# Kernel optimization log

Hardware: AMD Instinct MI355X
Metric: run time of the kernel (lower is better)

Reference implementation:

```python
import jax, jax.numpy as jnp
import numpy as np

B, S = 4, 1024
D = 256          # token_dim = channel_dim = expert_dim
D_LF = 768       # longformer hidden size
ADAPT = 128
NEXP = 4
HID = 64
DSUM = 3 * D + D_LF  # combiner concat width = 1536


def _gelu(v):
    return jax.nn.gelu(v, approximate=False)  # torch nn.GELU default = exact


def setup_inputs() -> dict:
    key = jax.random.key(0)
    ks = iter(jax.random.split(key, 40))
    def w(shape, scale=1.0):
        return jax.random.normal(next(ks), shape, jnp.float32) * scale
    z = lambda *shape: jnp.zeros(shape, jnp.float32)
    return dict(
        x=w((B, S, D)),
        lf_out=w((B, S, D_LF)),
        W_feat=w((D, ADAPT), D ** -0.5), b_feat=z(ADAPT),
        Wt=w((D, D), D ** -0.5), bt=z(D),
        Wt_a=w((ADAPT, D * D), 0.01 * ADAPT ** -0.5), bt_a=z(D * D),
        Wc=w((D, D), D ** -0.5), bc=z(D),
        Wc_a=w((ADAPT, D * D), 0.01 * ADAPT ** -0.5), bc_a=z(D * D),
        We=w((NEXP, D, D), D ** -0.5), be=z(NEXP, D),
        We_a=w((NEXP, ADAPT, D * D), 0.01 * ADAPT ** -0.5), be_a=z(NEXP, D * D),
        Wg=w((ADAPT, NEXP + 1), ADAPT ** -0.5), bg=z(NEXP + 1),
        Wphi=w((D, HID)), bphi=z(D, HID),
        Wpsi1=w((D * HID, HID), (D * HID) ** -0.5), bpsi1=z(HID),
        Wpsi2=w((HID, D), HID ** -0.5), bpsi2=z(D),
        Wres=w((DSUM, DSUM), DSUM ** -0.5), bres=z(DSUM),
        W1=w((DSUM, HID), DSUM ** -0.5), b1=z(HID),
        W2=w((HID, 4), HID ** -0.5), b2=z(4),
        Wo=w((DSUM, D), DSUM ** -0.5), bo=z(D),
    )


def reference(x, lf_out, W_feat, b_feat, Wt, bt, Wt_a, bt_a, Wc, bc, Wc_a, bc_a,
              We, be, We_a, be_a, Wg, bg, Wphi, bphi, Wpsi1, bpsi1, Wpsi2, bpsi2,
              Wres, bres, W1, b1, W2, b2, Wo, bo):
    Bx, Sx, d = x.shape
    N = Bx * Sx
    xf = x.reshape(N, d)
    lff = lf_out.reshape(N, -1)
    # featurizer -> per-token adapt features; global mean drives adaptive weights
    adapt = xf @ W_feat + b_feat            # [N, ADAPT]
    am = adapt.mean(axis=0)                 # [ADAPT] single adapt vector (LiquidLinear view constraint)

    def liquid(inp, Wb, bb, Wa, ba):
        Wdyn = Wb + (am @ Wa + ba).reshape(Wb.shape)
        return inp @ Wdyn + bb

    tok = liquid(xf, Wt, bt, Wt_a, bt_a)    # [N, D] token mixer
    chan = liquid(xf, Wc, bc, Wc_a, bc_a)   # [N, D] channel mixer

    # MixtureOfExperts: softmax gate over NEXP liquid experts + 1 KA expert
    gate = jax.nn.softmax(adapt @ Wg + bg, axis=-1)              # [N, NEXP+1]
    dW = (jnp.einsum('a,eaf->ef', am, We_a) + be_a).reshape(We.shape)
    eo = jnp.einsum('nd,edo->neo', xf, We + dW) + be[None]       # [N, E, D]
    # Kolmogorov-Arnold expert: per-feature phi (Linear(1,HID)+gelu), then psi MLP
    phi = _gelu(xf[:, :, None] * Wphi[None] + bphi[None])        # [N, D, HID]
    ka = _gelu(phi.reshape(N, -1) @ Wpsi1 + bpsi1) @ Wpsi2 + bpsi2
    moe = jnp.einsum('ne,ned->nd', gate[:, :-1], eo) + gate[:, -1:] * ka

    # ComponentCombination: learned softmax component weights + residual path
    concat = jnp.concatenate([tok, chan, moe, lff], axis=-1)     # [N, DSUM]
    residual = concat @ Wres + bres
    h = _gelu(concat @ W1 + b1)
    cw = jax.nn.softmax(h @ W2 + b2, axis=-1)                    # [N, 4]
    combined = jnp.concatenate(
        [cw[:, 0:1] * tok, cw[:, 1:2] * chan, cw[:, 2:3] * moe, cw[:, 3:4] * lff],
        axis=-1) + residual                                      # [N, DSUM]
    return (combined @ Wo + bo).reshape(Bx, Sx, d)
```

## Files before the change

### kernel.cpp

```cpp
#include <hip/hip_runtime.h>
#include <hip/hip_bf16.h>


__device__ __forceinline__ float gelu_f(float v){ return 0.5f*v*(1.0f + erff(v*0.70710678118654752f)); }

__device__ __forceinline__ float u16tof(unsigned short u){
  union { unsigned int i; float f; } v; v.i = ((unsigned int)u) << 16; return v.f;
}
__device__ __forceinline__ unsigned short f2b(float f){
  union { float f; unsigned int u; } v; v.f = f;
  unsigned int r = v.u + 0x7fffu + ((v.u >> 16) & 1u);
  return (unsigned short)(r >> 16);
}

using short8  = __attribute__((ext_vector_type(8))) short;
using float4v = __attribute__((ext_vector_type(4))) float;

template<int MODE>
__global__ __launch_bounds__(256) void mgemm_k(
    const unsigned short* __restrict__ A, const unsigned short* __restrict__ Bt,
    const float* __restrict__ bias, float* __restrict__ C,
    int M, int N, int K, long sB, long sBias, long sC)
{
  if constexpr (MODE==1){
    Bt   += sB   * blockIdx.z;
    bias += sBias* blockIdx.z;
    C    += sC   * blockIdx.z;
  }
  __shared__ __align__(16) unsigned short As[128][40];
  __shared__ __align__(16) unsigned short Bs[128][40];
  const int tid  = threadIdx.x;
  const int m0   = blockIdx.y*128, n0 = blockIdx.x*128;
  const int wave = tid>>6, lane = tid&63;
  const int wm   = (wave&1)*64, wn = (wave>>1)*64;
  const int q    = lane>>4, r = lane&15;
  const int sm   = tid>>2, sq = (tid&3)*8;

  float4v acc[4][4];
  #pragma unroll
  for (int i=0;i<4;i++)
    #pragma unroll
    for (int j=0;j<4;j++) acc[i][j] = (float4v){0.f,0.f,0.f,0.f};

  const unsigned short* Ap = A + (long)(m0+sm)*K + sq;
  const unsigned short* Bp = Bt + (long)(n0+sm)*K + sq;
  const long rstep = (long)64*K;

  for (int k0 = 0; k0 < K; k0 += 32){
    uint4 a0 = *(const uint4*)(Ap + k0);
    uint4 a1 = *(const uint4*)(Ap + k0 + rstep);
    uint4 b0 = *(const uint4*)(Bp + k0);
    uint4 b1 = *(const uint4*)(Bp + k0 + rstep);
    __syncthreads();
    *(uint4*)&As[sm   ][sq] = a0;
    *(uint4*)&As[sm+64][sq] = a1;
    *(uint4*)&Bs[sm   ][sq] = b0;
    *(uint4*)&Bs[sm+64][sq] = b1;
    __syncthreads();
    short8 af[4], bf[4];
    #pragma unroll
    for (int mt=0;mt<4;mt++) af[mt] = *(const short8*)&As[wm + mt*16 + r][q*8];
    #pragma unroll
    for (int nt=0;nt<4;nt++) bf[nt] = *(const short8*)&Bs[wn + nt*16 + r][q*8];
    #pragma unroll
    for (int mt=0;mt<4;mt++)
      #pragma unroll
      for (int nt=0;nt<4;nt++)
        acc[mt][nt] = __builtin_amdgcn_mfma_f32_16x16x32_bf16(af[mt], bf[nt], acc[mt][nt], 0, 0, 0);
  }

  #pragma unroll
  for (int nt=0;nt<4;nt++){
    int col = n0 + wn + nt*16 + r;
    float bb = bias[col];
    #pragma unroll
    for (int mt=0;mt<4;mt++){
      #pragma unroll
      for (int i=0;i<4;i++){
        int row = m0 + wm + mt*16 + q*4 + i;
        C[(long)row*N + col] = acc[mt][nt][i] + bb;
      }
    }
  }
}

__global__ __launch_bounds__(256) void cvtb_k(const float* __restrict__ in, unsigned short* __restrict__ out){
  int i = (blockIdx.x*256 + threadIdx.x)*4;
  float4 v = *(const float4*)(in + i);
  ushort4 o; o.x = f2b(v.x); o.y = f2b(v.y); o.z = f2b(v.z); o.w = f2b(v.w);
  *(ushort4*)(out + i) = o;
}

__global__ __launch_bounds__(256) void tconv_k(const float* __restrict__ in, unsigned short* __restrict__ out, int R, int C){
  __shared__ float t[64][65];
  const int tid = threadIdx.x;
  const int c0 = blockIdx.x*64, r0 = blockIdx.y*64;
  const int lr = tid>>2, lc0 = (tid&3)*16;
  #pragma unroll
  for (int i=0;i<4;i++){
    float4 v = *(const float4*)&in[(long)(r0+lr)*C + c0 + lc0 + i*4];
    t[lr][lc0+i*4+0]=v.x; t[lr][lc0+i*4+1]=v.y; t[lr][lc0+i*4+2]=v.z; t[lr][lc0+i*4+3]=v.w;
  }
  __syncthreads();
  const int oc = tid>>2, os = (tid&3)*16;
  #pragma unroll
  for (int i=0;i<16;i++)
    out[(long)(c0+oc)*R + r0 + os + i] = f2b(t[os+i][oc]);
}

__device__ __forceinline__ float4 ld4(const float* p){ return *(const float4*)p; }
__device__ __forceinline__ float4 ld4(const unsigned short* p){
  ushort4 u = *(const ushort4*)p;
  return make_float4(u16tof(u.x), u16tof(u.y), u16tof(u.z), u16tof(u.w));
}
template<typename AT, int MODE>
__global__ __launch_bounds__(256) void gemm_k(
    const AT* __restrict__ A, const float* __restrict__ B, const float* __restrict__ bias,
    float* __restrict__ C, int M, int N, int K, int Kc)
{
  int klo = 0, khi = K;
  if constexpr (MODE==2){ klo = blockIdx.z*Kc; khi = klo + Kc; }
  __shared__ __align__(16) float As[16][68];
  __shared__ __align__(16) float Bs[16][68];
  const int tid = threadIdx.x;
  const int m0 = blockIdx.y*64, n0 = blockIdx.x*64;
  const int ty = tid>>4, tx = tid&15;
  const int ar = tid>>2, ac = (tid&3)*4;
  const int kr = tid>>4, nc = (tid&15)*4;
  float acc[4][4] = {};
  const AT* Ap = A + (long)(m0+ar)*K;

  for (int k0 = klo; k0 < khi; k0 += 16){
    float4 av = ld4(Ap + k0 + ac);
    float4 bv = *(const float4*)(B + (long)(k0+kr)*N + (n0+nc));
    __syncthreads();
    As[ac+0][ar] = av.x; As[ac+1][ar] = av.y; As[ac+2][ar] = av.z; As[ac+3][ar] = av.w;
    *(float4*)&Bs[kr][nc] = bv;
    __syncthreads();
    #pragma unroll
    for (int k = 0; k < 16; k++){
      float4 a4 = *(const float4*)&As[k][ty*4];
      float4 b4 = *(const float4*)&Bs[k][tx*4];
      float a[4] = {a4.x,a4.y,a4.z,a4.w};
      float b[4] = {b4.x,b4.y,b4.z,b4.w};
      #pragma unroll
      for (int i = 0; i < 4; i++)
        #pragma unroll
        for (int j = 0; j < 4; j++)
          acc[i][j] = fmaf(a[i], b[j], acc[i][j]);
    }
  }
  float bv4[4];
  #pragma unroll
  for (int j = 0; j < 4; j++) bv4[j] = bias[n0 + tx*4 + j];
  #pragma unroll
  for (int i = 0; i < 4; i++){
    long row = m0 + ty*4 + i;
    #pragma unroll
    for (int j = 0; j < 4; j++){
      float v = acc[i][j];
      if constexpr (MODE==2){
        if (blockIdx.z == 0) v += bv4[j];
        atomicAdd(&C[row*(long)N + n0 + tx*4 + j], v);
      } else {
        C[row*(long)N + n0 + tx*4 + j] = v + bv4[j];
      }
    }
  }
}

__global__ __launch_bounds__(256) void colmean_k(const float* __restrict__ adapt, float* __restrict__ am){
  __shared__ float red[256];
  int a = blockIdx.x, tid = threadIdx.x;
  float s = 0.f;
  for (int n = tid; n < 4096; n += 256) s += adapt[n*128 + a];
  red[tid] = s; __syncthreads();
  for (int w = 128; w > 0; w >>= 1){ if (tid < w) red[tid] += red[tid+w]; __syncthreads(); }
  if (tid == 0) am[a] = red[0] * (1.0f/4096.0f);
}

__global__ __launch_bounds__(256) void gate_k(const float* __restrict__ adapt,
    const float* __restrict__ Wg, const float* __restrict__ bg, float* __restrict__ gate){
  __shared__ float wg[640]; __shared__ float bgs[5];
  int tid = threadIdx.x;
  for (int i = tid; i < 640; i += 256) wg[i] = Wg[i];
  if (tid < 5) bgs[tid] = bg[tid];
  __syncthreads();
  int n = blockIdx.x*256 + tid;
  float l[5] = {bgs[0],bgs[1],bgs[2],bgs[3],bgs[4]};
  const float* ar = adapt + (long)n*128;
  for (int a = 0; a < 128; a++){
    float av = ar[a];
    #pragma unroll
    for (int e = 0; e < 5; e++) l[e] = fmaf(av, wg[a*5+e], l[e]);
  }
  float mx = l[0];
  #pragma unroll
  for (int e = 1; e < 5; e++) mx = fmaxf(mx, l[e]);
  float sum = 0.f;
  #pragma unroll
  for (int e = 0; e < 5; e++){ l[e] = expf(l[e]-mx); sum += l[e]; }
  float inv = 1.0f/sum;
  #pragma unroll
  for (int e = 0; e < 5; e++) gate[(long)n*5+e] = l[e]*inv;
}

__global__ __launch_bounds__(256) void dynw_k(const float* __restrict__ am,
    const float* Wt, const float* Wt_a, const float* bt_a,
    const float* Wc, const float* Wc_a, const float* bc_a,
    const float* We, const float* We_a, const float* be_a,
    unsigned short* __restrict__ Wdyn_t)
{
  __shared__ float ams[128];
  int tid = threadIdx.x;
  if (tid < 128) ams[tid] = am[tid];
  __syncthreads();
  long gid = (long)blockIdx.x*256 + tid;
  int seg = (int)(gid >> 16); int m = (int)(gid & 65535);
  const float *W, *Wa, *ba;
  if (seg == 0){ W = Wt; Wa = Wt_a; ba = bt_a; }
  else if (seg == 1){ W = Wc; Wa = Wc_a; ba = bc_a; }
  else { int e = seg-2; W = We + (long)e*65536; Wa = We_a + (long)e*65536*128; ba = be_a + (long)e*65536; }
  float s = W[m] + ba[m];
  for (int a = 0; a < 128; a++) s = fmaf(ams[a], Wa[(long)a*65536 + m], s);
  int row = m >> 8, col = m & 255;
  Wdyn_t[(long)seg*65536 + (long)col*256 + row] = f2b(s);
}

__global__ void bias6_k(const float* bt, const float* bc, const float* be, float* bias6){
  int z = blockIdx.x, t = threadIdx.x;
  const float* s = (z==0) ? bt : (z==1) ? bc : be + (long)(z-2)*256;
  bias6[z*256 + t] = s[t];
}

__global__ __launch_bounds__(256) void psi1_k(const float* __restrict__ xf,
    const float* __restrict__ Wphi, const float* __restrict__ bphi,
    const float* __restrict__ Wpsi1, float* __restrict__ h1)
{
  __shared__ __align__(16) float xs[64][33];
  __shared__ __align__(16) float As[64][68];
  __shared__ __align__(16) float Bs[64][68];
  const int tid = threadIdx.x;
  const int m0 = blockIdx.x*64;
  const int d_lo = blockIdx.y*32;
  {
    int t = tid>>2, dq = (tid&3)*8;
    const float* src = xf + (long)(m0+t)*256 + d_lo + dq;
    #pragma unroll
    for (int i = 0; i < 8; i++) xs[t][dq+i] = src[i];
  }
  const int ty = tid>>4, tx = tid&15;
  const int k_a = tid>>2, t0_a = (tid&3)*16;
  float acc[4][4] = {};
  __syncthreads();
  for (int dd = 0; dd < 32; dd++){
    int d = d_lo + dd;
    const float* wp = Wpsi1 + (long)d*4096;
    float w  = Wphi[d*64 + k_a];
    float bb = bphi[d*64 + k_a];
    __syncthreads();
    #pragma unroll
    for (int i = 0; i < 16; i++){
      int idx = tid + 256*i;
      Bs[idx>>6][idx&63] = wp[idx];
    }
    #pragma unroll
    for (int i = 0; i < 16; i++){
      float xv = xs[t0_a+i][dd];
      As[k_a][t0_a+i] = gelu_f(fmaf(xv, w, bb));
    }
    __syncthreads();
    #pragma unroll
    for (int kk = 0; kk < 64; kk++){
      float4 a4 = *(const float4*)&As[kk][ty*4];
      float4 b4 = *(const float4*)&Bs[kk][tx*4];
      float a[4] = {a4.x,a4.y,a4.z,a4.w};
      float b[4] = {b4.x,b4.y,b4.z,b4.w};
      #pragma unroll
      for (int i = 0; i < 4; i++)
        #pragma unroll
        for (int j = 0; j < 4; j++)
          acc[i][j] = fmaf(a[i], b[j], acc[i][j]);
    }
  }
  #pragma unroll
  for (int i = 0; i < 4; i++)
    #pragma unroll
    for (int j = 0; j < 4; j++)
      atomicAdd(&h1[(long)(m0 + ty*4 + i)*64 + tx*4 + j], acc[i][j]);
}

__global__ __launch_bounds__(256) void h1g_k(const float* __restrict__ h1,
    const float* __restrict__ bpsi1, float* __restrict__ h1g){
  int i = blockIdx.x*256 + threadIdx.x;
  h1g[i] = gelu_f(h1[i] + bpsi1[i & 63]);
}

__global__ __launch_bounds__(256) void concat_k(const float* __restrict__ tok,
    const float* __restrict__ chan, const float* __restrict__ eo,
    const float* __restrict__ gate, const float* __restrict__ ka,
    const float* __restrict__ lf, unsigned short* __restrict__ concat)
{
  int n = blockIdx.x, tid = threadIdx.x;
  const float* g = gate + (long)n*5;
  float g0=g[0], g1=g[1], g2=g[2], g3=g[3], g4=g[4];
  long nb = (long)n*1536;
  int d = tid;
  concat[nb + d]        = f2b(tok[(long)n*256 + d]);
  concat[nb + 256 + d]  = f2b(chan[(long)n*256 + d]);
  float m = g0*eo[(long)n*256 + d]
          + g1*eo[1048576 + (long)n*256 + d]
          + g2*eo[2097152 + (long)n*256 + d]
          + g3*eo[3145728 + (long)n*256 + d]
          + g4*ka[(long)n*256 + d];
  concat[nb + 512 + d] = f2b(m);
  for (int j = tid; j < 768; j += 256) concat[nb + 768 + j] = f2b(lf[(long)n*768 + j]);
}

__global__ __launch_bounds__(256) void cw_k(const float* __restrict__ hpre,
    const float* __restrict__ W2, const float* __restrict__ b2, float* __restrict__ cw){
  __shared__ float w2s[256]; __shared__ float b2s[4];
  int tid = threadIdx.x;
  w2s[tid] = W2[tid];
  if (tid < 4) b2s[tid] = b2[tid];
  __syncthreads();
  int n = blockIdx.x*256 + tid;
  float l[4] = {b2s[0],b2s[1],b2s[2],b2s[3]};
  const float* hp = hpre + (long)n*64;
  for (int j = 0; j < 64; j++){
    float hj = gelu_f(hp[j]);
    #pragma unroll
    for (int c = 0; c < 4; c++) l[c] = fmaf(hj, w2s[j*4+c], l[c]);
  }
  float mx = fmaxf(fmaxf(l[0],l[1]), fmaxf(l[2],l[3]));
  float sum = 0.f;
  #pragma unroll
  for (int c = 0; c < 4; c++){ l[c] = expf(l[c]-mx); sum += l[c]; }
  float inv = 1.0f/sum;
  #pragma unroll
  for (int c = 0; c < 4; c++) cw[(long)n*4+c] = l[c]*inv;
}

__global__ __launch_bounds__(256) void combine_k(unsigned short* __restrict__ concat,
    const float* __restrict__ residual, const float* __restrict__ cw){
  int n = blockIdx.x;
  int j = blockIdx.y*256 + threadIdx.x;
  int seg = (j < 768) ? (j >> 8) : 3;
  long idx = (long)n*1536 + j;
  float v = fmaf(cw[(long)n*4 + seg], u16tof(concat[idx]), residual[idx]);
  concat[idx] = f2b(v);
}

extern "C" void kernel_launch(void* const* d_in, const int* in_sizes, int n_in,
                              void* d_out, int out_size, void* d_ws, size_t ws_size,
                              hipStream_t stream)
{
  const float* x      = (const float*)d_in[0];
  const float* lf     = (const float*)d_in[1];
  const float* W_feat = (const float*)d_in[2];
  const float* b_feat = (const float*)d_in[3];
  const float* Wt     = (const float*)d_in[4];
  const float* bt     = (const float*)d_in[5];
  const float* Wt_a   = (const float*)d_in[6];
  const float* bt_a   = (const float*)d_in[7];
  const float* Wc     = (const float*)d_in[8];
  const float* bc     = (const float*)d_in[9];
  const float* Wc_a   = (const float*)d_in[10];
  const float* bc_a   = (const float*)d_in[11];
  const float* We     = (const float*)d_in[12];
  const float* be     = (const float*)d_in[13];
  const float* We_a   = (const float*)d_in[14];
  const float* be_a   = (const float*)d_in[15];
  const float* Wg     = (const float*)d_in[16];
  const float* bg     = (const float*)d_in[17];
  const float* Wphi   = (const float*)d_in[18];
  const float* bphi   = (const float*)d_in[19];
  const float* Wpsi1  = (const float*)d_in[20];
  const float* bpsi1  = (const float*)d_in[21];
  const float* Wpsi2  = (const float*)d_in[22];
  const float* bpsi2  = (const float*)d_in[23];
  const float* Wres   = (const float*)d_in[24];
  const float* bres   = (const float*)d_in[25];
  const float* W1     = (const float*)d_in[26];
  const float* b1     = (const float*)d_in[27];
  const float* W2     = (const float*)d_in[28];
  const float* b2     = (const float*)d_in[29];
  const float* Wo     = (const float*)d_in[30];
  const float* bo     = (const float*)d_in[31];

  float* ws = (float*)d_ws;
  float* T      = ws;
  float* tok    = T;
  float* chan   = T + 1048576;
  float* eo     = T + 2*1048576;
  float* adapt  = T + 6*1048576;
  float* am     = adapt + 524288;
  float* gate   = am + 128;
  float* bias6  = gate + 20480;
  float* h1     = bias6 + 1536;
  float* h1g    = h1 + 262144;
  float* ka     = h1g + 262144;
  unsigned short* xb     = (unsigned short*)(ka + 1048576);
  unsigned short* Wdyn_t = xb + 1048576;
  unsigned short* Wres_t = Wdyn_t + 393216;
  unsigned short* Wo_t   = Wres_t + 2359296;
  unsigned short* concat = Wo_t + 393216;
  float* residual = T;
  float* hpre   = adapt;
  float* cw     = adapt + 262144;

  dim3 b256(256);

  cvtb_k<<<dim3(1024), b256, 0, stream>>>(x, xb);
  tconv_k<<<dim3(24,24), b256, 0, stream>>>(Wres, Wres_t, 1536, 1536);
  tconv_k<<<dim3(4,24),  b256, 0, stream>>>(Wo,   Wo_t,   1536, 256);

  gemm_k<float,0><<<dim3(2,64,1), b256, 0, stream>>>(x, W_feat, b_feat, adapt, 4096,128,256, 0);

  colmean_k<<<dim3(128), b256, 0, stream>>>(adapt, am);
  gate_k<<<dim3(16), b256, 0, stream>>>(adapt, Wg, bg, gate);

  dynw_k<<<dim3(1536), b256, 0, stream>>>(am, Wt,Wt_a,bt_a, Wc,Wc_a,bc_a, We,We_a,be_a, Wdyn_t);
  bias6_k<<<dim3(6), b256, 0, stream>>>(bt, bc, be, bias6);

  mgemm_k<1><<<dim3(2,32,6), b256, 0, stream>>>(xb, Wdyn_t, bias6, T, 4096,256,256, 65536,256,1048576);

  hipMemsetAsync(h1, 0, 262144*sizeof(float), stream);
  psi1_k<<<dim3(64,8), b256, 0, stream>>>(x, Wphi, bphi, Wpsi1, h1);
  h1g_k<<<dim3(1024), b256, 0, stream>>>(h1, bpsi1, h1g);
  gemm_k<float,0><<<dim3(4,64,1), b256, 0, stream>>>(h1g, Wpsi2, bpsi2, ka, 4096,256,64, 0);

  concat_k<<<dim3(4096), b256, 0, stream>>>(tok, chan, eo, gate, ka, lf, concat);

  mgemm_k<0><<<dim3(12,32,1), b256, 0, stream>>>(concat, Wres_t, bres, residual, 4096,1536,1536, 0,0,0);

  hipMemsetAsync(hpre, 0, 262144*sizeof(float), stream);
  gemm_k<unsigned short,2><<<dim3(1,64,8), b256, 0, stream>>>(concat, W1, b1, hpre, 4096,64,1536, 192);
  cw_k<<<dim3(16), b256, 0, stream>>>(hpre, W2, b2, cw);

  combine_k<<<dim3(4096,6), b256, 0, stream>>>(concat, residual, cw);

  mgemm_k<0><<<dim3(2,32,1), b256, 0, stream>>>(concat, Wo_t, bo, (float*)d_out, 4096,256,1536, 0,0,0);
}
```

Baseline: 744.0 us.

## Move KA psi1 GEMM to bf16 MFMA with transposed bf16 weight

Replaces the fp32 FMA-based fused phi+psi1 kernel with one that runs the inner products on bf16 MFMA 16x16x32 instructions. The Wpsi1 weight is transposed and converted to bf16 in an extra tconv launch, and Wphi/bphi are packed as bf16 pairs in shared memory. Each thread computes its GELU phi values before the barrier, overlapping them with the global weight loads. This is meant to cut the ALU cost of the largest fp32 GEMM (K=16384). In exchange it adds a conversion pass over Wpsi1 and bf16 rounding of the activations, weights and phi parameters.

```diff
diff --git a/kernel.cpp b/kernel.cpp
--- a/kernel.cpp
+++ b/kernel.cpp
@@ -81,6 +81,105 @@
         C[(long)row*N + col] = acc[mt][nt][i] + bb;
       }
     }
+  }
+}
+
+__global__ __launch_bounds__(256) void psi1m_k(const float* __restrict__ x,
+    const float* __restrict__ Wphi, const float* __restrict__ bphi,
+    const unsigned short* __restrict__ Wpsi1_t, float* __restrict__ h1)
+{
+  __shared__ float xs[64][33];
+  __shared__ __align__(16) unsigned int wbls[32][64];
+  __shared__ __align__(16) unsigned short As[64][72];
+  __shared__ __align__(16) unsigned short Bs[64][72];
+  const int tid = threadIdx.x;
+  const int m0 = blockIdx.x*64, d_lo = blockIdx.y*32;
+
+  {
+    int m = tid>>2, off = (tid&3)*8;
+    const float* src = x + (long)(m0+m)*256 + d_lo + off;
+    #pragma unroll
+    for (int i=0;i<8;i++) xs[m][off+i] = src[i];
+  }
+  {
+    #pragma unroll
+    for (int i=0;i<2;i++){
+      int idx4 = tid + 256*i;
+      int rr = idx4>>4, cc = (idx4&15)*4;
+      float4 w4 = *(const float4*)&Wphi[(long)(d_lo+rr)*64 + cc];
+      float4 b4 = *(const float4*)&bphi[(long)(d_lo+rr)*64 + cc];
+      uint4 p;
+      p.x = (unsigned int)f2b(w4.x) | ((unsigned int)f2b(b4.x)<<16);
+      p.y = (unsigned int)f2b(w4.y) | ((unsigned int)f2b(b4.y)<<16);
+      p.z = (unsigned int)f2b(w4.z) | ((unsigned int)f2b(b4.z)<<16);
+      p.w = (unsigned int)f2b(w4.w) | ((unsigned int)f2b(b4.w)<<16);
+      *(uint4*)&wbls[rr][cc] = p;
+    }
+  }
+  const int wave = tid>>6, lane = tid&63;
+  const int wm = (wave&1)*32, wn = (wave>>1)*32;
+  const int q = lane>>4, r = lane&15;
+  const int pm = tid>>2, pk = (tid&3)*16;
+  const int bn = tid>>2, bk = (tid&3)*16;
+
+  float4v acc[2][2];
+  #pragma unroll
+  for (int i=0;i<2;i++)
+    #pragma unroll
+    for (int j=0;j<2;j++) acc[i][j] = (float4v){0.f,0.f,0.f,0.f};
+
+  __syncthreads();
+
+  for (int dd=0; dd<32; dd++){
+    int dglob = d_lo + dd;
+    const unsigned short* wp = Wpsi1_t + (long)bn*16384 + (long)dglob*64 + bk;
+    uint4 b0 = *(const uint4*)wp;
+    uint4 b1 = *(const uint4*)(wp + 8);
+    float xv = xs[pm][dd];
+    ushort4 ph[4];
+    #pragma unroll
+    for (int kk=0; kk<4; kk++){
+      uint4 wb = *(const uint4*)&wbls[dd][pk + kk*4];
+      unsigned int u[4] = {wb.x, wb.y, wb.z, wb.w};
+      unsigned short o[4];
+      #pragma unroll
+      for (int e=0;e<4;e++){
+        float w = u16tof((unsigned short)(u[e] & 0xffffu));
+        float b = u16tof((unsigned short)(u[e] >> 16));
+        o[e] = f2b(gelu_f(fmaf(xv, w, b)));
+      }
+      ph[kk].x=o[0]; ph[kk].y=o[1]; ph[kk].z=o[2]; ph[kk].w=o[3];
+    }
+    __syncthreads();
+    *(uint4*)&Bs[bn][bk]   = b0;
+    *(uint4*)&Bs[bn][bk+8] = b1;
+    #pragma unroll
+    for (int kk=0;kk<4;kk++) *(ushort4*)&As[pm][pk+kk*4] = ph[kk];
+    __syncthreads();
+    #pragma unroll
+    for (int kb=0; kb<2; kb++){
+      short8 af[2], bfr[2];
+      #pragma unroll
+      for (int mt=0;mt<2;mt++) af[mt]  = *(const short8*)&As[wm+mt*16+r][kb*32 + q*8];
+      #pragma unroll
+      for (int nt=0;nt<2;nt++) bfr[nt] = *(const short8*)&Bs[wn+nt*16+r][kb*32 + q*8];
+      #pragma unroll
+      for (int mt=0;mt<2;mt++)
+        #pragma unroll
+        for (int nt=0;nt<2;nt++)
+          acc[mt][nt] = __builtin_amdgcn_mfma_f32_16x16x32_bf16(af[mt], bfr[nt], acc[mt][nt], 0, 0, 0);
+    }
+  }
+  #pragma unroll
+  for (int nt=0;nt<2;nt++){
+    int col = wn + nt*16 + r;
+    #pragma unroll
+    for (int mt=0;mt<2;mt++)
+      #pragma unroll
+      for (int i=0;i<4;i++){
+        int row = m0 + wm + mt*16 + q*4 + i;
+        atomicAdd(&h1[(long)row*64 + col], acc[mt][nt][i]);
+      }
   }
 }
 
@@ -231,63 +330,6 @@
   int z = blockIdx.x, t = threadIdx.x;
   const float* s = (z==0) ? bt : (z==1) ? bc : be + (long)(z-2)*256;
   bias6[z*256 + t] = s[t];
-}
-
-__global__ __launch_bounds__(256) void psi1_k(const float* __restrict__ xf,
-    const float* __restrict__ Wphi, const float* __restrict__ bphi,
-    const float* __restrict__ Wpsi1, float* __restrict__ h1)
-{
-  __shared__ __align__(16) float xs[64][33];
-  __shared__ __align__(16) float As[64][68];
-  __shared__ __align__(16) float Bs[64][68];
-  const int tid = threadIdx.x;
-  const int m0 = blockIdx.x*64;
-  const int d_lo = blockIdx.y*32;
-  {
-    int t = tid>>2, dq = (tid&3)*8;
-    const float* src = xf + (long)(m0+t)*256 + d_lo + dq;
-    #pragma unroll
-    for (int i = 0; i < 8; i++) xs[t][dq+i] = src[i];
-  }
-  const int ty = tid>>4, tx = tid&15;
-  const int k_a = tid>>2, t0_a = (tid&3)*16;
-  float acc[4][4] = {};
-  __syncthreads();
-  for (int dd = 0; dd < 32; dd++){
-    int d = d_lo + dd;
-    const float* wp = Wpsi1 + (long)d*4096;
-    float w  = Wphi[d*64 + k_a];
-    float bb = bphi[d*64 + k_a];
-    __syncthreads();
-    #pragma unroll
-    for (int i = 0; i < 16; i++){
-      int idx = tid + 256*i;
-      Bs[idx>>6][idx&63] = wp[idx];
-    }
-    #pragma unroll
-    for (int i = 0; i < 16; i++){
-      float xv = xs[t0_a+i][dd];
-      As[k_a][t0_a+i] = gelu_f(fmaf(xv, w, bb));
-    }
-    __syncthreads();
-    #pragma unroll
-    for (int kk = 0; kk < 64; kk++){
-      float4 a4 = *(const float4*)&As[kk][ty*4];
-      float4 b4 = *(const float4*)&Bs[kk][tx*4];
-      float a[4] = {a4.x,a4.y,a4.z,a4.w};
-      float b[4] = {b4.x,b4.y,b4.z,b4.w};
-      #pragma unroll
-      for (int i = 0; i < 4; i++)
-        #pragma unroll
-        for (int j = 0; j < 4; j++)
-          acc[i][j] = fmaf(a[i], b[j], acc[i][j]);
-    }
-  }
-  #pragma unroll
-  for (int i = 0; i < 4; i++)
-    #pragma unroll
-    for (int j = 0; j < 4; j++)
-      atomicAdd(&h1[(long)(m0 + ty*4 + i)*64 + tx*4 + j], acc[i][j]);
 }
 
 __global__ __launch_bounds__(256) void h1g_k(const float* __restrict__ h1,
@@ -400,11 +442,12 @@
   float* h1     = bias6 + 1536;
   float* h1g    = h1 + 262144;
   float* ka     = h1g + 262144;
-  unsigned short* xb     = (unsigned short*)(ka + 1048576);
-  unsigned short* Wdyn_t = xb + 1048576;
-  unsigned short* Wres_t = Wdyn_t + 393216;
-  unsigned short* Wo_t   = Wres_t + 2359296;
-  unsigned short* concat = Wo_t + 393216;
+  unsigned short* xb      = (unsigned short*)(ka + 1048576);
+  unsigned short* Wdyn_t  = xb + 1048576;
+  unsigned short* Wres_t  = Wdyn_t + 393216;
+  unsigned short* Wo_t    = Wres_t + 2359296;
+  unsigned short* Wpsi1_t = Wo_t + 393216;
+  unsigned short* concat  = Wpsi1_t + 1048576;
   float* residual = T;
   float* hpre   = adapt;
   float* cw     = adapt + 262144;
@@ -414,6 +457,7 @@
   cvtb_k<<<dim3(1024), b256, 0, stream>>>(x, xb);
   tconv_k<<<dim3(24,24), b256, 0, stream>>>(Wres, Wres_t, 1536, 1536);
   tconv_k<<<dim3(4,24),  b256, 0, stream>>>(Wo,   Wo_t,   1536, 256);
+  tconv_k<<<dim3(1,256), b256, 0, stream>>>(Wpsi1, Wpsi1_t, 16384, 64);
 
   gemm_k<float,0><<<dim3(2,64,1), b256, 0, stream>>>(x, W_feat, b_feat, adapt, 4096,128,256, 0);
 
@@ -426,7 +470,7 @@
   mgemm_k<1><<<dim3(2,32,6), b256, 0, stream>>>(xb, Wdyn_t, bias6, T, 4096,256,256, 65536,256,1048576);
 
   hipMemsetAsync(h1, 0, 262144*sizeof(float), stream);
-  psi1_k<<<dim3(64,8), b256, 0, stream>>>(x, Wphi, bphi, Wpsi1, h1);
+  psi1m_k<<<dim3(64,8), b256, 0, stream>>>(x, Wphi, bphi, Wpsi1_t, h1);
   h1g_k<<<dim3(1024), b256, 0, stream>>>(h1, bpsi1, h1g);
   gemm_k<float,0><<<dim3(4,64,1), b256, 0, stream>>>(h1g, Wpsi2, bpsi2, ka, 4096,256,64, 0);
 
```

New measurement: 627.0 us. -15.7%, faster.
